# Kernel optimization log

Measured on AMD Instinct MI355X. Metric: run time of the kernel, lower is better.

Reference implementation:

```python
import jax, jax.numpy as jnp
import numpy as np

D_MODEL = 1024
NUM_HEADS = 16
D_HEAD = 64  # d_q = d_k = d_v
BATCH = 4
SEQ = 2048


def _trunc_normal(key, shape, std):
    # truncated normal in [-3*std, 3*std], matching nn.init.trunc_normal_
    return jax.random.truncated_normal(key, -3.0, 3.0, shape, dtype=jnp.float32) * std


def setup_inputs() -> dict:
    key = jax.random.key(0)
    k_x, k_q, k_k, k_v, k_o = jax.random.split(key, 5)
    hd = NUM_HEADS * D_HEAD
    s_in = np.sqrt(2.0 / (D_MODEL + hd))
    s_out = np.sqrt(2.0 / (hd + D_MODEL))
    return {
        "in_features": jax.random.normal(k_x, (BATCH, SEQ, D_MODEL), dtype=jnp.float32),
        "w_q": _trunc_normal(k_q, (hd, D_MODEL), s_in),
        "w_k": _trunc_normal(k_k, (hd, D_MODEL), s_in),
        "w_v": _trunc_normal(k_v, (hd, D_MODEL), s_in),
        "w_o": _trunc_normal(k_o, (D_MODEL, hd), s_out),
    }


def reference(in_features, w_q, w_k, w_v, w_o):
    B, S, D = in_features.shape
    H, Dh = NUM_HEADS, D_HEAD
    # QKV projections (weight stored as [out, in])
    q = jnp.einsum('od,bsd->bso', w_q, in_features).reshape(B, S, H, Dh).transpose(0, 2, 1, 3)
    k = jnp.einsum('od,bsd->bso', w_k, in_features).reshape(B, S, H, Dh).transpose(0, 2, 1, 3)
    v = jnp.einsum('od,bsd->bso', w_v, in_features).reshape(B, S, H, Dh).transpose(0, 2, 1, 3)
    # scaled dot-product attention with dense causal mask (as in source)
    att = jnp.einsum('bhqd,bhkd->bhqk', q, k) / jnp.sqrt(jnp.float32(Dh)).astype(q.dtype)
    causal = jnp.tril(jnp.ones((S, S), dtype=bool))
    att = jnp.where(causal, att, -jnp.inf)
    att = jax.nn.softmax(att, axis=-1)
    out = jnp.einsum('bhqk,bhkd->bhqd', att, v)  # [B,H,S,Dh]
    out = out.transpose(0, 2, 1, 3).reshape(B, S, H * Dh)
    return jnp.einsum('od,bsd->bso', w_o, out)
```

## Files before the change

### kernel.cpp

```cpp
#include <hip/hip_runtime.h>
#include <stdint.h>

#define D_MODEL 1024
#define NHEADS  16
#define DHEAD   64
#define BATCH   4
#define SEQ     2048
#define MTOT    (BATCH*SEQ)

typedef unsigned short u16;
typedef uint32_t u32;
typedef __bf16 bf16x8 __attribute__((ext_vector_type(8)));
typedef float  f32x4  __attribute__((ext_vector_type(4)));
typedef float  f32x16 __attribute__((ext_vector_type(16)));
typedef u16    u16x8  __attribute__((ext_vector_type(8)));
typedef u16    u16x4  __attribute__((ext_vector_type(4)));
typedef u32    u32x4  __attribute__((ext_vector_type(4)));

__device__ __forceinline__ u16 f2bf(float f) {
  uint32_t u = __builtin_bit_cast(uint32_t, f);
  u += 0x7fff + ((u >> 16) & 1);
  return (u16)(u >> 16);
}

__device__ __forceinline__ void gll16(const u16* g, u16* lds) {
  __builtin_amdgcn_global_load_lds(
      (__attribute__((address_space(1))) void*)(g),
      (__attribute__((address_space(3))) void*)(lds), 16, 0, 0);
}

__global__ void cvtk(const float4* __restrict__ in, u16x4* __restrict__ out, int n4) {
  const int i = blockIdx.x * blockDim.x + threadIdx.x;
  if (i < n4) {
    const float4 f = in[i];
    u16x4 h;
    h[0] = f2bf(f.x); h[1] = f2bf(f.y); h[2] = f2bf(f.z); h[3] = f2bf(f.w);
    out[i] = h;
  }
}

__global__ void cvtk4(const float4* __restrict__ a, const float4* __restrict__ b,
                      const float4* __restrict__ c, const float4* __restrict__ d,
                      u16x4* __restrict__ out, int n4) {
  const int i = blockIdx.x * blockDim.x + threadIdx.x;
  if (i >= n4) return;
  const float4* src = (blockIdx.y == 0) ? a : (blockIdx.y == 1) ? b
                    : (blockIdx.y == 2) ? c : d;
  const float4 f = src[i];
  u16x4 h;
  h[0] = f2bf(f.x); h[1] = f2bf(f.y); h[2] = f2bf(f.z); h[3] = f2bf(f.w);
  out[(size_t)blockIdx.y * n4 + i] = h;
}

template<int MODE>
__launch_bounds__(256)
__global__ void gemm_bt_k(const u16* __restrict__ A,
                          const u16* __restrict__ W0,
                          const u16* __restrict__ W1,
                          const u16* __restrict__ W2,
                          void* __restrict__ Cout)
{
  constexpr int K = D_MODEL;
  const int tid = threadIdx.x;
  const int l = tid & 63, w = tid >> 6;
  const int m0 = blockIdx.x * 128;
  const int n0 = blockIdx.y * 128;
  const u16* Bm = W0;
  float scale = 1.0f;
  if (MODE == 1) {
    const int z = blockIdx.z;
    Bm = (z == 0) ? W0 : ((z == 1) ? W1 : W2);
    scale = (z == 0) ? 0.125f * 1.44269504088896f : 1.0f;
  }

  __shared__ __align__(16) u16 As[128*32];
  __shared__ __align__(16) u16 Bs[128*32];

  f32x4 acc[4][4];
  #pragma unroll
  for (int i = 0; i < 4; ++i)
    #pragma unroll
    for (int j = 0; j < 4; ++j)
      acc[i][j] = f32x4{0.f, 0.f, 0.f, 0.f};

  const int wr = w >> 1, wc = w & 1;
  const int srow = l >> 2;
  const int scol = (l & 3) * 8;

  for (int k0 = 0; k0 < K; k0 += 32) {
    __syncthreads();
    #pragma unroll
    for (int j = 0; j < 2; ++j) {
      const int seg = w * 2 + j;
      gll16(A  + (size_t)(m0 + seg*16 + srow) * K + k0 + scol, &As[seg*512]);
      gll16(Bm + (size_t)(n0 + seg*16 + srow) * K + k0 + scol, &Bs[seg*512]);
    }
    __syncthreads();
    bf16x8 af[4], bfr[4];
    #pragma unroll
    for (int m = 0; m < 4; ++m)
      af[m] = *(const bf16x8*)&As[(wr*64 + m*16 + (l & 15))*32 + (l >> 4)*8];
    #pragma unroll
    for (int n = 0; n < 4; ++n)
      bfr[n] = *(const bf16x8*)&Bs[(wc*64 + n*16 + (l & 15))*32 + (l >> 4)*8];
    #pragma unroll
    for (int m = 0; m < 4; ++m)
      #pragma unroll
      for (int n = 0; n < 4; ++n)
        acc[m][n] = __builtin_amdgcn_mfma_f32_16x16x32_bf16(af[m], bfr[n], acc[m][n], 0, 0, 0);
  }

  const int g = l >> 4, c15 = l & 15;
  #pragma unroll
  for (int m = 0; m < 4; ++m) {
    #pragma unroll
    for (int n = 0; n < 4; ++n) {
      #pragma unroll
      for (int j = 0; j < 4; ++j) {
        const int row = m0 + wr*64 + m*16 + g*4 + j;
        const int col = n0 + wc*64 + n*16 + c15;
        const float v = acc[m][n][j] * scale;
        if (MODE == 0) {
          ((float*)Cout)[(size_t)row * D_MODEL + col] = v;
        } else {
          const int b = row >> 11, s = row & (SEQ-1);
          const int h = col >> 6, dh = col & (DHEAD-1);
          ((u16*)Cout)[(size_t)blockIdx.z * MTOT * D_MODEL
                       + ((size_t)(b*NHEADS + h) * SEQ + s) * DHEAD + dh] = f2bf(v);
        }
      }
    }
  }
}

__launch_bounds__(512, 2)
__global__ void attn6_k(const u16* __restrict__ Qb, const u16* __restrict__ Kb_,
                        const u16* __restrict__ Vb_, u16* __restrict__ Oa)
{
  const int tid = threadIdx.x;
  const int w = tid >> 6, l = tid & 63;
  const int q5 = l & 31, hi = l >> 5;
  const int r = blockIdx.x;
  const int bh = (r & 7) * 8 + ((r >> 3) & 7);
  const int pairi = r >> 6;
  const int b = bh >> 4, h = bh & 15;
  const size_t base = (size_t)bh * SEQ * DHEAD;
  const u16* Qg = Qb + base;
  const u16* Kg = Kb_ + base;
  const u16* Vg = Vb_ + base;

  __shared__ __align__(16) u16 smem[32768];

  const int kc = tid & 7, rp = tid >> 3;
  const int vsub = rp >> 5;
  const int rp5 = rp & 31;
  int vIdx32[8];
  #pragma unroll
  for (int e = 0; e < 8; ++e)
    vIdx32[e] = vsub*2048 + (8*kc + e)*32 + ((((rp5 >> 2) ^ kc ^ e) & 7) << 2) + (rp5 & 3);

  const int kr8 = l >> 3;
  const int kkv = 8*w + kr8;
  const int kdc = (l & 7) ^ kr8 ^ w;

  for (int half = 0; half < 2; ++half) {
    const int tq = half ? (7 - pairi) : pairi;
    const int q0w = tq*256 + 32*w;
    const int ntk = (tq + 1) * 2;
    const int ntw = (q0w >> 7) + 1;

    bf16x8 qf[4];
    #pragma unroll
    for (int s = 0; s < 4; ++s)
      qf[s] = *(const bf16x8*)(Qg + (size_t)(q0w + q5)*DHEAD + 16*s + 8*hi);

    f32x16 c0 = {}, c1 = {};
    float mrun = -1e30f, lrun = 0.f;

    {
      #pragma unroll
      for (int h2 = 0; h2 < 2; ++h2)
        gll16(Kg + (size_t)(64*h2 + kkv)*DHEAD + kdc*8, smem + h2*4096 + w*512);
      const u16x8 v0 = *(const u16x8*)(Vg + (size_t)(2*rp)*DHEAD + kc*8);
      const u16x8 v1 = *(const u16x8*)(Vg + (size_t)(2*rp + 1)*DHEAD + kc*8);
      u32* Vd = (u32*)(smem + 16384);
      #pragma unroll
      for (int e = 0; e < 8; ++e)
        Vd[vIdx32[e]] = (u32)v0[e] | ((u32)v1[e] << 16);
    }
    __syncthreads();

    for (int t = 0; t < ntk; ++t) {
      const int cur = t & 1;
      const bool pf = (t + 1 < ntk);
      u16x8 v0, v1;
      if (pf) {
        const int kv1 = (t + 1) * 128;
        v0 = *(const u16x8*)(Vg + (size_t)(kv1 + 2*rp)*DHEAD + kc*8);
        v1 = *(const u16x8*)(Vg + (size_t)(kv1 + 2*rp + 1)*DHEAD + kc*8);
        #pragma unroll
        for (int h2 = 0; h2 < 2; ++h2)
          gll16(Kg + (size_t)(kv1 + 64*h2 + kkv)*DHEAD + kdc*8,
                smem + (cur^1)*8192 + h2*4096 + w*512);
      }

      if (t < ntw) {
        const u16* Kb = smem + cur*8192;
        const u16* Vv = smem + 16384 + cur*8192;

        f32x16 st[4] = {{}, {}, {}, {}};
        __builtin_amdgcn_s_setprio(1);
        #pragma unroll
        for (int kbg = 0; kbg < 4; ++kbg) {
          #pragma unroll
          for (int s = 0; s < 4; ++s) {
            const int slot = ((2*s + hi) ^ (l & 7) ^ ((4*(kbg & 1)) & 7) ^ (q5 >> 3)) & 7;
            const bf16x8 kf = *(const bf16x8*)(Kb + (kbg >> 1)*4096
                                               + ((kbg & 1)*32 + q5)*64 + slot*8);
            st[kbg] = __builtin_amdgcn_mfma_f32_32x32x16_bf16(kf, qf[s], st[kbg], 0, 0, 0);
          }
        }
        __builtin_amdgcn_s_setprio(0);

        if (t == ntw - 1) {
          const int kv0 = t * 128;
          #pragma unroll
          for (int kbg = 0; kbg < 4; ++kbg)
            #pragma unroll
            for (int rr = 0; rr < 16; ++rr) {
              const int kvg = kv0 + 32*kbg + (rr & 3) + 8*(rr >> 2) + 4*hi;
              if (kvg > q0w + q5) st[kbg][rr] = -1e30f;
            }
        }

        float mx = -1e30f;
        #pragma unroll
        for (int kbg = 0; kbg < 4; ++kbg)
          #pragma unroll
          for (int rr = 0; rr < 16; ++rr) mx = fmaxf(mx, st[kbg][rr]);
        mx = fmaxf(mx, __shfl_xor(mx, 32));
        float alpha = 1.0f;
        if (!__all(mx <= mrun + 8.0f)) {
          const float mnew = fmaxf(mrun, mx);
          alpha = __builtin_amdgcn_exp2f(mrun - mnew);
          mrun = mnew;
          #pragma unroll
          for (int rr = 0; rr < 16; ++rr) { c0[rr] *= alpha; c1[rr] *= alpha; }
        }
        float rs = 0.f;
        #pragma unroll
        for (int kbg = 0; kbg < 4; ++kbg)
          #pragma unroll
          for (int rr = 0; rr < 16; ++rr) {
            const float pe = __builtin_amdgcn_exp2f(st[kbg][rr] - mrun);
            st[kbg][rr] = pe;
            rs += pe;
          }
        rs += __shfl_xor(rs, 32);
        lrun = lrun * alpha + rs;

        bf16x8 pb[8];
        #pragma unroll
        for (int kbg = 0; kbg < 4; ++kbg) {
          u32 pw[8];
          #pragma unroll
          for (int i = 0; i < 8; ++i) {
            u32 t0;
            asm("v_cvt_pk_bf16_f32 %0, %1, %2"
                : "=v"(t0) : "v"(st[kbg][2*i]), "v"(st[kbg][2*i+1]));
            pw[i] = t0;
          }
          asm("v_permlane32_swap_b32 %0, %1" : "+v"(pw[0]), "+v"(pw[2]));
          asm("v_permlane32_swap_b32 %0, %1" : "+v"(pw[1]), "+v"(pw[3]));
          asm("v_permlane32_swap_b32 %0, %1" : "+v"(pw[4]), "+v"(pw[6]));
          asm("v_permlane32_swap_b32 %0, %1" : "+v"(pw[5]), "+v"(pw[7]));
          pb[2*kbg]   = __builtin_bit_cast(bf16x8, u32x4{pw[0], pw[1], pw[2], pw[3]});
          pb[2*kbg+1] = __builtin_bit_cast(bf16x8, u32x4{pw[4], pw[5], pw[6], pw[7]});
        }

        __builtin_amdgcn_s_setprio(1);
        #pragma unroll
        for (int h2 = 0; h2 < 2; ++h2) {
          #pragma unroll
          for (int s = 0; s < 4; ++s) {
            {
              const int slot = ((2*s + hi) ^ (l & 7) ^ (q5 >> 3)) & 7;
              const bf16x8 vf = *(const bf16x8*)(Vv + h2*4096 + q5*64 + slot*8);
              c0 = __builtin_amdgcn_mfma_f32_32x32x16_bf16(vf, pb[4*h2 + s], c0, 0, 0, 0);
            }
            {
              const int slot = ((2*s + hi) ^ (l & 7) ^ 4 ^ (q5 >> 3)) & 7;
              const bf16x8 vf = *(const bf16x8*)(Vv + h2*4096 + (32 + q5)*64 + slot*8);
              c1 = __builtin_amdgcn_mfma_f32_32x32x16_bf16(vf, pb[4*h2 + s], c1, 0, 0, 0);
            }
          }
        }
        __builtin_amdgcn_s_setprio(0);
      }

      if (pf) {
        u32* Vd = (u32*)(smem + 16384) + (cur^1)*4096;
        #pragma unroll
        for (int e = 0; e < 8; ++e)
          Vd[vIdx32[e]] = (u32)v0[e] | ((u32)v1[e] << 16);
      }
      __syncthreads();
    }

    const float linv = __builtin_amdgcn_rcpf(lrun);
    #pragma unroll
    for (int Ab = 0; Ab < 2; ++Ab)
      #pragma unroll
      for (int rr = 0; rr < 16; ++rr) {
        const int d = 32*Ab + (rr & 3) + 8*(rr >> 2) + 4*hi;
        smem[w*2048 + q5*64 + (((d >> 3) ^ (q5 & 7)) & 7)*8 + (d & 7)] =
            f2bf((Ab ? c1[rr] : c0[rr]) * linv);
      }
    __syncthreads();
    #pragma unroll
    for (int cc = 0; cc < 4; ++cc) {
      const int dchunk = 4*hi + cc;
      const u16x8 vv = *(const u16x8*)&smem[w*2048 + q5*64 + ((dchunk ^ (q5 & 7)) & 7)*8];
      *(u16x8*)(Oa + (size_t)(b*SEQ + q0w + q5)*D_MODEL + h*DHEAD + 32*hi + 8*cc) = vv;
    }
    __syncthreads();
  }
}

extern "C" void kernel_launch(void* const* d_in, const int* in_sizes, int n_in,
                              void* d_out, int out_size, void* d_ws, size_t ws_size,
                              hipStream_t stream) {
  const float* X  = (const float*)d_in[0];
  const float* Wq = (const float*)d_in[1];
  const float* Wk = (const float*)d_in[2];
  const float* Wv = (const float*)d_in[3];
  const float* Wo = (const float*)d_in[4];

  u16* xb  = (u16*)d_ws;
  u16* wqb = xb  + (size_t)MTOT*D_MODEL;
  u16* wkb = wqb + (size_t)D_MODEL*D_MODEL;
  u16* wvb = wkb + (size_t)D_MODEL*D_MODEL;
  u16* wob = wvb + (size_t)D_MODEL*D_MODEL;
  u16* qkv = wob + (size_t)D_MODEL*D_MODEL;
  u16* att = qkv + (size_t)3*MTOT*D_MODEL;

  const int nx4 = MTOT*D_MODEL/4;
  const int nw4 = D_MODEL*D_MODEL/4;
  cvtk<<<nx4/256, 256, 0, stream>>>((const float4*)X, (u16x4*)xb, nx4);
  dim3 gc(nw4/256, 4, 1);
  cvtk4<<<gc, 256, 0, stream>>>((const float4*)Wq, (const float4*)Wk,
                                (const float4*)Wv, (const float4*)Wo,
                                (u16x4*)wqb, nw4);

  dim3 g1(MTOT/128, D_MODEL/128, 3);
  gemm_bt_k<1><<<g1, 256, 0, stream>>>(xb, wqb, wkb, wvb, (void*)qkv);

  attn6_k<<<256, 512, 0, stream>>>(qkv, qkv + (size_t)MTOT*D_MODEL,
                                   qkv + (size_t)2*MTOT*D_MODEL, att);

  dim3 g3(MTOT/128, D_MODEL/128, 1);
  gemm_bt_k<0><<<g3, 256, 0, stream>>>(att, wob, nullptr, nullptr, d_out);
}
```

Baseline: 162.1 us.

## Replace QKV projection with 256x256-tile multistage pipelined GEMM using direct global-to-LDS loads

Replaces the 128x128-tile QKV projection (three grid slices, one per weight) with a single 256x256-tile kernel over a concatenated 3072-wide weight. It uses a 4-slot LDS ring filled by asynchronous global-to-LDS loads (gll16) with swizzled columns, explicit vmcnt waits, and raised MFMA priority. A bijective block-index remap groups tiles for L2 reuse. This targets global-memory latency and LDS bank conflicts in the old synchronous single-buffer loop. The cost is 128KB of dynamic shared memory, which relies on the existing gll16 helper and on wqb/wkb/wvb being contiguous.

```diff
diff --git a/kernel.cpp b/kernel.cpp
--- a/kernel.cpp
+++ b/kernel.cpp
@@ -50,6 +50,110 @@
   u16x4 h;
   h[0] = f2bf(f.x); h[1] = f2bf(f.y); h[2] = f2bf(f.z); h[3] = f2bf(f.w);
   out[(size_t)blockIdx.y * n4 + i] = h;
+}
+
+#define QSLOT 16384
+
+__global__ __launch_bounds__(512, 2) void gemm_qkv8(
+    const u16* __restrict__ A, const u16* __restrict__ Bw, u16* __restrict__ Out)
+{
+  extern __shared__ u16 qsm[];
+  const int tid = threadIdx.x;
+  const int w = tid >> 6, l = tid & 63;
+  const int wm = w >> 2, wn = w & 3;
+  const int bid = blockIdx.x;
+  const int wg = (bid & 7) * 48 + (bid >> 3);
+  const int m0 = (wg / 12) * 256, n0 = (wg % 12) * 256;
+
+  const int srow = l >> 2;
+  const int sc   = (l & 3) ^ ((l >> 3) & 3);
+  const int nA0 = w * 2, nA1 = w * 2 + 1;
+  const u16* gA0 = A  + (size_t)(m0 + nA0*16 + srow) * 1024 + sc*8;
+  const u16* gA1 = A  + (size_t)(m0 + nA1*16 + srow) * 1024 + sc*8;
+  const u16* gB0 = Bw + (size_t)(n0 + nA0*16 + srow) * 1024 + sc*8;
+  const u16* gB1 = Bw + (size_t)(n0 + nA1*16 + srow) * 1024 + sc*8;
+
+  const int cp = ((l >> 4) ^ ((l >> 1) & 3)) * 8;
+  const int ra = wm * 128 + (l & 15);
+  const int rb = wn * 64 + (l & 15);
+
+  f32x4 acc[8][4];
+  #pragma unroll
+  for (int i = 0; i < 8; ++i)
+    #pragma unroll
+    for (int j = 0; j < 4; ++j)
+      acc[i][j] = f32x4{0.f, 0.f, 0.f, 0.f};
+
+#define QSTAGE(slot, s) do {                                          \
+    gll16(gA0 + (s)*32, qsm + (slot)*QSLOT + nA0*512);                \
+    gll16(gA1 + (s)*32, qsm + (slot)*QSLOT + nA1*512);                \
+    gll16(gB0 + (s)*32, qsm + (slot)*QSLOT + 8192 + nA0*512);         \
+    gll16(gB1 + (s)*32, qsm + (slot)*QSLOT + 8192 + nA1*512);         \
+  } while (0)
+
+#define QCOMP(slot) do {                                                        \
+    const u16* As_ = qsm + (slot)*QSLOT;                                        \
+    const u16* Bs_ = As_ + 8192;                                                \
+    bf16x8 af[8], bfr[4];                                                       \
+    _Pragma("unroll")                                                           \
+    for (int mf = 0; mf < 8; ++mf)                                              \
+      af[mf] = *(const bf16x8*)&As_[(ra + mf*16)*32 + cp];                      \
+    _Pragma("unroll")                                                           \
+    for (int nf = 0; nf < 4; ++nf)                                              \
+      bfr[nf] = *(const bf16x8*)&Bs_[(rb + nf*16)*32 + cp];                     \
+    __builtin_amdgcn_s_setprio(1);                                              \
+    _Pragma("unroll")                                                           \
+    for (int mf = 0; mf < 8; ++mf)                                              \
+      _Pragma("unroll")                                                         \
+      for (int nf = 0; nf < 4; ++nf)                                            \
+        acc[mf][nf] = __builtin_amdgcn_mfma_f32_16x16x32_bf16(af[mf], bfr[nf],  \
+                                                              acc[mf][nf], 0, 0, 0); \
+    __builtin_amdgcn_s_setprio(0);                                              \
+  } while (0)
+
+  QSTAGE(0, 0);
+  QSTAGE(1, 1);
+  asm volatile("s_waitcnt vmcnt(4)" ::: "memory");
+  __builtin_amdgcn_s_barrier();
+  __builtin_amdgcn_sched_barrier(0);
+
+  #pragma unroll 2
+  for (int s = 0; s < 30; ++s) {
+    QSTAGE((s + 2) & 3, s + 2);
+    QCOMP(s & 3);
+    asm volatile("s_waitcnt vmcnt(4)" ::: "memory");
+    __builtin_amdgcn_s_barrier();
+    __builtin_amdgcn_sched_barrier(0);
+  }
+  QCOMP(2);
+  asm volatile("s_waitcnt vmcnt(0)" ::: "memory");
+  __builtin_amdgcn_s_barrier();
+  __builtin_amdgcn_sched_barrier(0);
+  QCOMP(3);
+
+#undef QSTAGE
+#undef QCOMP
+
+  const float scale = (n0 < 1024) ? 0.125f * 1.44269504088896f : 1.0f;
+  const int g = l >> 4, c15 = l & 15;
+  #pragma unroll
+  for (int mf = 0; mf < 8; ++mf) {
+    #pragma unroll
+    for (int nf = 0; nf < 4; ++nf) {
+      #pragma unroll
+      for (int j = 0; j < 4; ++j) {
+        const int row = m0 + wm*128 + mf*16 + g*4 + j;
+        const int col = n0 + wn*64 + nf*16 + c15;
+        const int z = col >> 10;
+        const int wi = col & 1023;
+        const int b = row >> 11, sq = row & (SEQ-1);
+        const int h = wi >> 6, dh = wi & (DHEAD-1);
+        Out[(size_t)z * MTOT * D_MODEL
+            + ((size_t)(b*NHEADS + h) * SEQ + sq) * DHEAD + dh] =
+            f2bf(acc[mf][nf][j] * scale);
+      }
+    }
+  }
 }
 
 template<int MODE>
@@ -66,12 +170,6 @@
   const int m0 = blockIdx.x * 128;
   const int n0 = blockIdx.y * 128;
   const u16* Bm = W0;
-  float scale = 1.0f;
-  if (MODE == 1) {
-    const int z = blockIdx.z;
-    Bm = (z == 0) ? W0 : ((z == 1) ? W1 : W2);
-    scale = (z == 0) ? 0.125f * 1.44269504088896f : 1.0f;
-  }
 
   __shared__ __align__(16) u16 As[128*32];
   __shared__ __align__(16) u16 Bs[128*32];
@@ -119,15 +217,7 @@
       for (int j = 0; j < 4; ++j) {
         const int row = m0 + wr*64 + m*16 + g*4 + j;
         const int col = n0 + wc*64 + n*16 + c15;
-        const float v = acc[m][n][j] * scale;
-        if (MODE == 0) {
-          ((float*)Cout)[(size_t)row * D_MODEL + col] = v;
-        } else {
-          const int b = row >> 11, s = row & (SEQ-1);
-          const int h = col >> 6, dh = col & (DHEAD-1);
-          ((u16*)Cout)[(size_t)blockIdx.z * MTOT * D_MODEL
-                       + ((size_t)(b*NHEADS + h) * SEQ + s) * DHEAD + dh] = f2bf(v);
-        }
+        ((float*)Cout)[(size_t)row * D_MODEL + col] = acc[m][n][j];
       }
     }
   }
@@ -344,6 +434,9 @@
   u16* qkv = wob + (size_t)D_MODEL*D_MODEL;
   u16* att = qkv + (size_t)3*MTOT*D_MODEL;
 
+  (void)hipFuncSetAttribute((const void*)gemm_qkv8,
+                            hipFuncAttributeMaxDynamicSharedMemorySize, 131072);
+
   const int nx4 = MTOT*D_MODEL/4;
   const int nw4 = D_MODEL*D_MODEL/4;
   cvtk<<<nx4/256, 256, 0, stream>>>((const float4*)X, (u16x4*)xb, nx4);
@@ -352,8 +445,7 @@
                                 (const float4*)Wv, (const float4*)Wo,
                                 (u16x4*)wqb, nw4);
 
-  dim3 g1(MTOT/128, D_MODEL/128, 3);
-  gemm_bt_k<1><<<g1, 256, 0, stream>>>(xb, wqb, wkb, wvb, (void*)qkv);
+  gemm_qkv8<<<384, 512, 131072, stream>>>(xb, wqb, qkv);
 
   attn6_k<<<256, 512, 0, stream>>>(qkv, qkv + (size_t)MTOT*D_MODEL,
                                    qkv + (size_t)2*MTOT*D_MODEL, att);
```

New measurement: 162.2 us. No clear change (+0.0%).
